# Kernel optimization log

Measured on AMD Instinct MI355X. Metric: run time of the kernel, lower is better.

## Reference

```python
import jax, jax.numpy as jnp
import numpy as np

B, C = 8192, 4096

def setup_inputs() -> dict:
    key = jax.random.key(0)
    k0, k1, k2, k3 = jax.random.split(key, 4)
    x = jax.random.normal(k0, (B, C), dtype=jnp.float32)
    target = jax.random.randint(k1, (B,), 0, C, dtype=jnp.int32)
    # distance_rank[t] is the list of class indices ranked by wordnet distance
    # from class t; emulate with a random permutation per row.
    scores = jax.random.uniform(k2, (C, C))
    distance_rank = jnp.argsort(scores, axis=1).astype(jnp.int32)
    # k = randint(class_index + 1, class_num - 1) inclusive, per (batch, class_index)
    c = jnp.arange(2, C - 1)  # class_index values, [C-3]
    span = (C - 1) - (c + 1) + 1  # number of valid k values per class_index
    u = jax.random.uniform(k3, (B, C - 3))
    k_idx = (c + 1 + jnp.floor(u * span)).astype(jnp.int32)
    k_idx = jnp.minimum(k_idx, C - 1)
    return {"x": x, "target": target, "distance_rank": distance_rank, "k_idx": k_idx}


def reference(x, target, distance_rank, k_idx):
    Bn, Cn = x.shape
    alpha = jnp.float32(Cn - 1)  # len(input[0]) - 1
    ranks = distance_rank[target]  # [B, C] class ids ranked by distance from target
    yi = jnp.take_along_axis(x, ranks[:, 1:2], axis=1)        # [B, 1]
    yj = jnp.take_along_axis(x, ranks[:, 2:Cn - 1], axis=1)   # [B, C-3]
    yk_cls = jnp.take_along_axis(ranks, k_idx, axis=1)        # [B, C-3]
    yk = jnp.take_along_axis(x, yk_cls, axis=1)               # [B, C-3]
    # mid = (1 + (yi - y)^2/alpha)^(-(alpha+1)/2); computed in log space for
    # stability (exponent is -(C)/2, direct pow underflows)
    e = -(alpha + 1.0) / 2.0
    la = e * jnp.log1p((yi - yj) ** 2 / alpha)
    lb = e * jnp.log1p((yi - yk) ** 2 / alpha)
    # log2(pijk) = (log midij - log(midij + midik)) / ln 2
    log2_pijk = (la - jnp.logaddexp(la, lb)) / jnp.log(jnp.float32(2.0))
    ctste = jnp.sum(log2_pijk)
    sc = -ctste / Bn / (Cn - 1)
    # F.cross_entropy(input, target), mean reduction
    logp = jax.nn.log_softmax(x, axis=1)
    ce = -jnp.mean(jnp.take_along_axis(logp, target[:, None], axis=1))
    theta = jnp.float32(0.6)
    return theta * ce + (1.0 - theta) * sc
```

## Files before the change

kernel.cpp:

```cpp
#include <hip/hip_runtime.h>
#include <math.h>

constexpr int BN  = 8192;
constexpr int CN  = 4096;
constexpr int NT  = 256;
constexpr int NW  = NT / 64;
constexpr int EPT = CN / NT;
constexpr int V4  = EPT / 4;

__global__ __launch_bounds__(NT) void sc_row_kernel(
    const float* __restrict__ x,
    const int*   __restrict__ target,
    const int*   __restrict__ distance_rank,
    const int*   __restrict__ k_idx,
    float*       __restrict__ ws)
{
    __shared__ float xs[CN];
    __shared__ float red_m[NW], red_s[NW], red_a[NW];

    const int b    = blockIdx.x;
    const int tid  = threadIdx.x;
    const int lane = tid & 63;
    const int wave = tid >> 6;

    const int t = target[b];
    const float* __restrict__ xrow = x + (size_t)b * CN;
    const int*   __restrict__ drow = distance_rank + (size_t)t * CN;
    const int*   __restrict__ krow = k_idx + (size_t)b * (CN - 3);

    int rkv[EPT];
    #pragma unroll
    for (int i = 0; i < EPT; ++i) rkv[i] = drow[tid + i * NT];
    const int rk1 = drow[1];

    float4 xv[V4];
    #pragma unroll
    for (int i = 0; i < V4; ++i) {
        xv[i] = reinterpret_cast<const float4*>(xrow)[tid + i * NT];
        reinterpret_cast<float4*>(xs)[tid + i * NT] = xv[i];
    }

    float ml = -__builtin_huge_valf();
    #pragma unroll
    for (int i = 0; i < V4; ++i) {
        ml = fmaxf(ml, fmaxf(fmaxf(xv[i].x, xv[i].y), fmaxf(xv[i].z, xv[i].w)));
    }
    float sl = 0.f;
    #pragma unroll
    for (int i = 0; i < V4; ++i) {
        sl += __expf(xv[i].x - ml) + __expf(xv[i].y - ml)
            + __expf(xv[i].z - ml) + __expf(xv[i].w - ml);
    }
    #pragma unroll
    for (int off = 32; off; off >>= 1) {
        const float mo = __shfl_down(ml, off, 64);
        const float so = __shfl_down(sl, off, 64);
        const float mn = fmaxf(ml, mo);
        sl = sl * __expf(ml - mn) + so * __expf(mo - mn);
        ml = mn;
    }
    if (lane == 0) { red_m[wave] = ml; red_s[wave] = sl; }

    __syncthreads();

    float mg = red_m[0];
    #pragma unroll
    for (int w = 1; w < NW; ++w) mg = fmaxf(mg, red_m[w]);
    float sg = 0.f;
    #pragma unroll
    for (int w = 0; w < NW; ++w) sg += red_s[w] * __expf(red_m[w] - mg);

    if (tid == 0) ws[BN + b] = __logf(sg) + mg - xs[t];

    const float yi = xs[rk1];
    float yv[EPT];
    #pragma unroll
    for (int i = 0; i < EPT; ++i) yv[i] = xs[rkv[i]];

    __syncthreads();

    const float alpha = (float)(CN - 1);
    const float e     = -0.5f * (float)CN;
    int kkv[EPT];
    #pragma unroll
    for (int i = 0; i < EPT; ++i) {
        const int c = tid + i * NT;
        const float d = yi - yv[i];
        xs[c] = __log2f(fmaf(d, d, alpha));
        kkv[i] = (c < CN - 3) ? krow[c] : 3;
    }
    __syncthreads();

    float acc = 0.f;
    #pragma unroll
    for (int i = 0; i < EPT; ++i) {
        const int j = tid + i * NT;
        const float Lj = xs[(j < CN - 3) ? (2 + j) : 0];
        const float Lk = xs[kkv[i]];
        const float D  = e * (Lk - Lj);
        const float term = fmaxf(D, 0.f)
                         + __log2f(1.0f + __builtin_amdgcn_exp2f(-fabsf(D)));
        acc -= (j < CN - 3) ? term : 0.f;
    }

    #pragma unroll
    for (int off = 32; off; off >>= 1) acc += __shfl_down(acc, off, 64);
    if (lane == 0) red_a[wave] = acc;
    __syncthreads();
    if (tid == 0) {
        float a0 = red_a[0];
        #pragma unroll
        for (int w = 1; w < NW; ++w) a0 += red_a[w];
        ws[b] = a0;
    }
}

__global__ __launch_bounds__(1024) void sc_finalize(
    const float* __restrict__ ws, float* __restrict__ out)
{
    __shared__ double dred[32];
    const int tid  = threadIdx.x;
    const int lane = tid & 63;
    const int wave = tid >> 6;

    double sc = 0.0, ce = 0.0;
    for (int i = tid; i < BN; i += 1024) {
        sc += (double)ws[i];
        ce += (double)ws[BN + i];
    }
    for (int off = 32; off; off >>= 1) {
        sc += __shfl_down(sc, off, 64);
        ce += __shfl_down(ce, off, 64);
    }
    if (lane == 0) { dred[wave] = sc; dred[16 + wave] = ce; }
    __syncthreads();
    if (tid == 0) {
        double scs = 0.0, ces = 0.0;
        #pragma unroll
        for (int w = 0; w < 16; ++w) { scs += dred[w]; ces += dred[16 + w]; }
        double ce_mean = ces / (double)BN;
        double sc_val  = -scs / (double)BN / (double)(CN - 1);
        out[0] = (float)(0.6 * ce_mean + 0.4 * sc_val);
    }
}

extern "C" void kernel_launch(void* const* d_in, const int* in_sizes, int n_in,
                              void* d_out, int out_size, void* d_ws, size_t ws_size,
                              hipStream_t stream) {
    const float* x             = (const float*)d_in[0];
    const int*   target        = (const int*)d_in[1];
    const int*   distance_rank = (const int*)d_in[2];
    const int*   k_idx         = (const int*)d_in[3];
    float*       ws            = (float*)d_ws;

    sc_row_kernel<<<BN, NT, 0, stream>>>(x, target, distance_rank, k_idx, ws);
    sc_finalize<<<1, 1024, 0, stream>>>(ws, (float*)d_out);
}
```

Baseline: 67.99 us.

## Process multiple rows per block with double-buffered async LDS staging

Each block now handles 8 consecutive rows with 512 threads. While the current row is being processed, the next row's x values are staged into a second shared buffer with asynchronous global-to-LDS loads, and its distance_rank row is prefetched into registers. The j-side log terms are kept in registers rather than re-read from shared memory. The aim is to hide load latency behind compute in a bandwidth-bound kernel. In exchange, the block count drops, register pressure rises, and correctness depends on the async LDS loads having completed before the barriers.

```diff
diff --git a/kernel.cpp b/kernel.cpp
--- a/kernel.cpp
+++ b/kernel.cpp
@@ -1,117 +1,141 @@
 #include <hip/hip_runtime.h>
 #include <math.h>
 
-constexpr int BN  = 8192;
-constexpr int CN  = 4096;
-constexpr int NT  = 256;
-constexpr int NW  = NT / 64;
-constexpr int EPT = CN / NT;
-constexpr int V4  = EPT / 4;
+constexpr int BN   = 8192;
+constexpr int CN   = 4096;
+constexpr int NT   = 512;
+constexpr int NW   = NT / 64;
+constexpr int EPT  = CN / NT;
+constexpr int ROWS = 8;
+constexpr int GRID = BN / ROWS;
 
-__global__ __launch_bounds__(NT) void sc_row_kernel(
+__device__ __forceinline__ void stage_row(const float* __restrict__ gsrc,
+                                          float* ldst, int tid) {
+    #pragma unroll
+    for (int i = 0; i < CN / (NT * 4); ++i) {
+        const float* s = gsrc + (size_t)(tid + i * NT) * 4;
+        float*       d = ldst + (size_t)(tid + i * NT) * 4;
+        __builtin_amdgcn_global_load_lds(
+            (const __attribute__((address_space(1))) void*)s,
+            (__attribute__((address_space(3))) void*)d, 16, 0, 0);
+    }
+}
+
+__global__ __launch_bounds__(NT, 8) void sc_row_kernel(
     const float* __restrict__ x,
     const int*   __restrict__ target,
     const int*   __restrict__ distance_rank,
     const int*   __restrict__ k_idx,
     float*       __restrict__ ws)
 {
-    __shared__ float xs[CN];
+    __shared__ float xs[2][CN];
     __shared__ float red_m[NW], red_s[NW], red_a[NW];
 
-    const int b    = blockIdx.x;
     const int tid  = threadIdx.x;
     const int lane = tid & 63;
     const int wave = tid >> 6;
+    const int b0   = blockIdx.x * ROWS;
 
-    const int t = target[b];
-    const float* __restrict__ xrow = x + (size_t)b * CN;
-    const int*   __restrict__ drow = distance_rank + (size_t)t * CN;
-    const int*   __restrict__ krow = k_idx + (size_t)b * (CN - 3);
-
+    int t_cur = target[b0];
+    stage_row(x + (size_t)b0 * CN, xs[0], tid);
+    const int* dr0 = distance_rank + (size_t)t_cur * CN;
     int rkv[EPT];
     #pragma unroll
-    for (int i = 0; i < EPT; ++i) rkv[i] = drow[tid + i * NT];
-    const int rk1 = drow[1];
-
-    float4 xv[V4];
-    #pragma unroll
-    for (int i = 0; i < V4; ++i) {
-        xv[i] = reinterpret_cast<const float4*>(xrow)[tid + i * NT];
-        reinterpret_cast<float4*>(xs)[tid + i * NT] = xv[i];
-    }
-
-    float ml = -__builtin_huge_valf();
-    #pragma unroll
-    for (int i = 0; i < V4; ++i) {
-        ml = fmaxf(ml, fmaxf(fmaxf(xv[i].x, xv[i].y), fmaxf(xv[i].z, xv[i].w)));
-    }
-    float sl = 0.f;
-    #pragma unroll
-    for (int i = 0; i < V4; ++i) {
-        sl += __expf(xv[i].x - ml) + __expf(xv[i].y - ml)
-            + __expf(xv[i].z - ml) + __expf(xv[i].w - ml);
-    }
-    #pragma unroll
-    for (int off = 32; off; off >>= 1) {
-        const float mo = __shfl_down(ml, off, 64);
-        const float so = __shfl_down(sl, off, 64);
-        const float mn = fmaxf(ml, mo);
-        sl = sl * __expf(ml - mn) + so * __expf(mo - mn);
-        ml = mn;
-    }
-    if (lane == 0) { red_m[wave] = ml; red_s[wave] = sl; }
-
+    for (int i = 0; i < EPT; ++i) rkv[i] = dr0[tid + i * NT];
+    int rk1 = dr0[1];
     __syncthreads();
 
-    float mg = red_m[0];
-    #pragma unroll
-    for (int w = 1; w < NW; ++w) mg = fmaxf(mg, red_m[w]);
-    float sg = 0.f;
-    #pragma unroll
-    for (int w = 0; w < NW; ++w) sg += red_s[w] * __expf(red_m[w] - mg);
+    for (int r = 0; r < ROWS; ++r) {
+        const int cur = r & 1;
+        const int b   = b0 + r;
+        float* X = xs[cur];
 
-    if (tid == 0) ws[BN + b] = __logf(sg) + mg - xs[t];
+        int rkvN[EPT], rk1N = 0, tN = 0;
+        if (r + 1 < ROWS) {
+            tN = target[b + 1];
+            stage_row(x + (size_t)(b + 1) * CN, xs[cur ^ 1], tid);
+            const int* drN = distance_rank + (size_t)tN * CN;
+            #pragma unroll
+            for (int i = 0; i < EPT; ++i) rkvN[i] = drN[tid + i * NT];
+            rk1N = drN[1];
+        }
+        const int* krow = k_idx + (size_t)b * (CN - 3);
+        int kkv[EPT];
+        #pragma unroll
+        for (int i = 0; i < EPT; ++i) {
+            const int c  = tid + i * NT;
+            const int jj = (c < 2) ? 0 : ((c > CN - 2) ? (CN - 4) : (c - 2));
+            kkv[i] = krow[jj];
+        }
 
-    const float yi = xs[rk1];
-    float yv[EPT];
-    #pragma unroll
-    for (int i = 0; i < EPT; ++i) yv[i] = xs[rkv[i]];
+        float4 v0 = reinterpret_cast<float4*>(X)[tid];
+        float4 v1 = reinterpret_cast<float4*>(X)[tid + NT];
+        float ml = fmaxf(fmaxf(fmaxf(v0.x, v0.y), fmaxf(v0.z, v0.w)),
+                         fmaxf(fmaxf(v1.x, v1.y), fmaxf(v1.z, v1.w)));
+        float sl = __expf(v0.x-ml)+__expf(v0.y-ml)+__expf(v0.z-ml)+__expf(v0.w-ml)
+                 + __expf(v1.x-ml)+__expf(v1.y-ml)+__expf(v1.z-ml)+__expf(v1.w-ml);
+        #pragma unroll
+        for (int off = 32; off; off >>= 1) {
+            const float mo = __shfl_down(ml, off, 64);
+            const float so = __shfl_down(sl, off, 64);
+            const float mn = fmaxf(ml, mo);
+            sl = sl * __expf(ml - mn) + so * __expf(mo - mn);
+            ml = mn;
+        }
+        if (lane == 0) { red_m[wave] = ml; red_s[wave] = sl; }
 
-    __syncthreads();
+        const float xt = X[t_cur];
+        const float yi = X[rk1];
+        float yv[EPT];
+        #pragma unroll
+        for (int i = 0; i < EPT; ++i) yv[i] = X[rkv[i]];
 
-    const float alpha = (float)(CN - 1);
-    const float e     = -0.5f * (float)CN;
-    int kkv[EPT];
-    #pragma unroll
-    for (int i = 0; i < EPT; ++i) {
-        const int c = tid + i * NT;
-        const float d = yi - yv[i];
-        xs[c] = __log2f(fmaf(d, d, alpha));
-        kkv[i] = (c < CN - 3) ? krow[c] : 3;
-    }
-    __syncthreads();
+        __syncthreads();
 
-    float acc = 0.f;
-    #pragma unroll
-    for (int i = 0; i < EPT; ++i) {
-        const int j = tid + i * NT;
-        const float Lj = xs[(j < CN - 3) ? (2 + j) : 0];
-        const float Lk = xs[kkv[i]];
-        const float D  = e * (Lk - Lj);
-        const float term = fmaxf(D, 0.f)
-                         + __log2f(1.0f + __builtin_amdgcn_exp2f(-fabsf(D)));
-        acc -= (j < CN - 3) ? term : 0.f;
-    }
+        float mg = red_m[0];
+        #pragma unroll
+        for (int w = 1; w < NW; ++w) mg = fmaxf(mg, red_m[w]);
+        float sg = 0.f;
+        #pragma unroll
+        for (int w = 0; w < NW; ++w) sg += red_s[w] * __expf(red_m[w] - mg);
+        if (tid == 0) ws[BN + b] = __logf(sg) + mg - xt;
 
-    #pragma unroll
-    for (int off = 32; off; off >>= 1) acc += __shfl_down(acc, off, 64);
-    if (lane == 0) red_a[wave] = acc;
-    __syncthreads();
-    if (tid == 0) {
-        float a0 = red_a[0];
+        const float alpha = (float)(CN - 1);
+        float Lq[EPT];
         #pragma unroll
-        for (int w = 1; w < NW; ++w) a0 += red_a[w];
-        ws[b] = a0;
+        for (int i = 0; i < EPT; ++i) {
+            const int   c = tid + i * NT;
+            const float d = yi - yv[i];
+            Lq[i] = __log2f(fmaf(d, d, alpha));
+            X[c]  = Lq[i];
+        }
+        __syncthreads();
+
+        const float e = -0.5f * (float)CN;
+        float acc = 0.f;
+        #pragma unroll
+        for (int i = 0; i < EPT; ++i) {
+            const int   c  = tid + i * NT;
+            const float Lk = X[kkv[i]];
+            const float D  = e * (Lk - Lq[i]);
+            const float term = fmaxf(D, 0.f)
+                + __log2f(1.0f + __builtin_amdgcn_exp2f(-fabsf(D)));
+            acc -= (c >= 2 && c <= CN - 2) ? term : 0.f;
+        }
+        #pragma unroll
+        for (int off = 32; off; off >>= 1) acc += __shfl_down(acc, off, 64);
+        if (lane == 0) red_a[wave] = acc;
+        __syncthreads();
+        if (tid == 0) {
+            float a0 = red_a[0];
+            #pragma unroll
+            for (int w = 1; w < NW; ++w) a0 += red_a[w];
+            ws[b] = a0;
+        }
+
+        t_cur = tN; rk1 = rk1N;
+        #pragma unroll
+        for (int i = 0; i < EPT; ++i) rkv[i] = rkvN[i];
     }
 }
 
@@ -153,6 +177,6 @@
     const int*   k_idx         = (const int*)d_in[3];
     float*       ws            = (float*)d_ws;
 
-    sc_row_kernel<<<BN, NT, 0, stream>>>(x, target, distance_rank, k_idx, ws);
+    sc_row_kernel<<<GRID, NT, 0, stream>>>(x, target, distance_rank, k_idx, ws);
     sc_finalize<<<1, 1024, 0, stream>>>(ws, (float*)d_out);
 }
```

New measurement: 94.91 us. 1.4x slower.
